# Kernel optimization log

Measured on AMD Instinct MI355X. Metric: run time of the kernel, lower is better.

Reference implementation:

```python
import jax, jax.numpy as jnp
import numpy as np

B, T, C, H = 4, 2048, 1024, 16
D = C // H  # head dim = 64

def setup_inputs() -> dict:
    key = jax.random.key(0)
    k1, k2, k3 = jax.random.split(key, 3)
    x = jax.random.normal(k1, (B, T, C), dtype=jnp.float32)
    # torch Linear weight [out,in]; store transposed for x @ W
    W_attn = jax.random.normal(k2, (C, 3 * C), dtype=jnp.float32) * (1.0 / np.sqrt(C))
    W_proj = jax.random.normal(k3, (C, C), dtype=jnp.float32) * (1.0 / np.sqrt(C))
    return {"x": x, "W_attn": W_attn, "W_proj": W_proj}

def reference(x, W_attn, W_proj):
    qkv = x @ W_attn                          # [B,T,3C]
    q, k, v = jnp.split(qkv, 3, axis=-1)
    # [B,T,C] -> [B,H,T,D]
    def heads(t):
        return t.reshape(B, T, H, D).transpose(0, 2, 1, 3)
    q, k, v = heads(q), heads(k), heads(v)
    att = jnp.einsum('bhqd,bhkd->bhqk', q, k) * (1.0 / np.sqrt(D))  # [B,H,T,T]
    causal = jnp.tril(jnp.ones((T, T), dtype=bool))
    att = jnp.where(causal[None, None, :, :], att, -jnp.inf)
    att = jax.nn.softmax(att, axis=-1)
    y = jnp.einsum('bhqk,bhkd->bhqd', att, v)  # [B,H,T,D]
    y = y.transpose(0, 2, 1, 3).reshape(B, T, C)
    return y @ W_proj
```

## Files before the change

kernel.cpp:

```cpp
#include <hip/hip_runtime.h>
#include <hip/hip_bf16.h>

#define BB 4
#define TT 2048
#define CC 1024
#define HH 16
#define DD 64
#define MM (BB*TT)

typedef unsigned short u16;
typedef __bf16 bf16x8 __attribute__((ext_vector_type(8)));
typedef __bf16 bf16x4v __attribute__((ext_vector_type(4)));
typedef u16 u16x8 __attribute__((ext_vector_type(8)));
typedef u16 u16x4 __attribute__((ext_vector_type(4)));
typedef float f32x4 __attribute__((ext_vector_type(4)));

__device__ __forceinline__ u16 f2bf(float f) {
  union { float f; unsigned u; } v; v.f = f;
  unsigned u = v.u;
  return (u16)((u + 0x7fffu + ((u >> 16) & 1u)) >> 16);
}
__device__ __forceinline__ float bf2f(u16 s) {
  union { unsigned u; float f; } v; v.u = ((unsigned)s) << 16; return v.f;
}
__device__ __forceinline__ bf16x8 ld_bf16x8(const u16* p) {
  return *reinterpret_cast<const bf16x8*>(p);
}
__device__ __forceinline__ f32x4 zero4() {
  f32x4 z; z[0] = 0.f; z[1] = 0.f; z[2] = 0.f; z[3] = 0.f; return z;
}

__device__ __forceinline__ void gld_lds16(const u16* g, u16* l) {
  __builtin_amdgcn_global_load_lds(
      (const __attribute__((address_space(1))) void*)g,
      (__attribute__((address_space(3))) void*)l, 16, 0, 0);
}
__device__ __forceinline__ void wait_vm0() { __builtin_amdgcn_s_waitcnt(0x0F70); }

__device__ __forceinline__ float lane_pull(float x, int srclane) {
  int r = __builtin_amdgcn_ds_bpermute(srclane << 2, __builtin_bit_cast(int, x));
  return __builtin_bit_cast(float, r);
}

__global__ void k_cast_bf16(const float* __restrict__ x, u16* __restrict__ o, int n4) {
  int i = blockIdx.x * blockDim.x + threadIdx.x;
  if (i >= n4) return;
  const float4 v = reinterpret_cast<const float4*>(x)[i];
  u16x4 r; r.x = f2bf(v.x); r.y = f2bf(v.y); r.z = f2bf(v.z); r.w = f2bf(v.w);
  reinterpret_cast<u16x4*>(o)[i] = r;
}

__global__ void k_transpose_bf16(const float* __restrict__ W, u16* __restrict__ Wt,
                                 int K, int N) {
  __shared__ float tile[32][33];
  int nb = blockIdx.x * 32, kb = blockIdx.y * 32;
  int tx = threadIdx.x & 31, ty = threadIdx.x >> 5;
  #pragma unroll
  for (int i = ty; i < 32; i += 8)
    tile[i][tx] = W[(size_t)(kb + i) * N + nb + tx];
  __syncthreads();
  #pragma unroll
  for (int i = ty; i < 32; i += 8)
    Wt[(size_t)(nb + i) * K + kb + tx] = f2bf(tile[tx][i]);
}

template<int EPI>
__global__ __launch_bounds__(256, 3)
void k_gemm_bt(const u16* __restrict__ A, const u16* __restrict__ Bt,
               float* __restrict__ outF, u16* __restrict__ qb, u16* __restrict__ kb,
               u16* __restrict__ vt, int N, int K)
{
  __shared__ u16 As[128 * 64];
  __shared__ u16 Bs[128 * 64];
  const int tid  = threadIdx.x;
  const int lane = tid & 63, w = tid >> 6;
  const int l16  = lane & 15, quad = lane >> 4;
  const int wr = w >> 1, wc = w & 1;
  const int m0 = blockIdx.y * 128, n0 = blockIdx.x * 128;
  const int lr8 = lane >> 3, lc8 = lane & 7;

  f32x4 acc[4][4];
  #pragma unroll
  for (int i = 0; i < 4; ++i)
    #pragma unroll
    for (int j = 0; j < 4; ++j) acc[i][j] = zero4();

  for (int k0 = 0; k0 < K; k0 += 64) {
    __syncthreads();
    #pragma unroll
    for (int p = 0; p < 4; ++p) {
      const int row = w * 32 + p * 8 + lr8;
      const int cs  = lc8 ^ (row & 7);
      gld_lds16(A  + (size_t)(m0 + row) * K + k0 + cs * 8, &As[(w * 32 + p * 8) * 64]);
      gld_lds16(Bt + (size_t)(n0 + row) * K + k0 + cs * 8, &Bs[(w * 32 + p * 8) * 64]);
    }
    wait_vm0();
    __syncthreads();
    #pragma unroll
    for (int s = 0; s < 2; ++s) {
      bf16x8 af[4], bfr[4];
      #pragma unroll
      for (int i = 0; i < 4; ++i) {
        int mrow = wr * 64 + i * 16 + l16;
        af[i]  = ld_bf16x8(&As[mrow * 64 + ((s * 4 + quad) ^ (l16 & 7)) * 8]);
        int nrow = wc * 64 + i * 16 + l16;
        bfr[i] = ld_bf16x8(&Bs[nrow * 64 + ((s * 4 + quad) ^ (l16 & 7)) * 8]);
      }
      #pragma unroll
      for (int i = 0; i < 4; ++i)
        #pragma unroll
        for (int j = 0; j < 4; ++j)
          acc[i][j] = __builtin_amdgcn_mfma_f32_16x16x32_bf16(af[i], bfr[j], acc[i][j], 0, 0, 0);
    }
  }

  #pragma unroll
  for (int i = 0; i < 4; ++i) {
    #pragma unroll
    for (int j = 0; j < 4; ++j) {
      const int n = n0 + wc * 64 + j * 16 + l16;
      const int mb = m0 + wr * 64 + i * 16 + quad * 4;
      if (EPI == 0) {
        #pragma unroll
        for (int r = 0; r < 4; ++r)
          outF[(size_t)(mb + r) * N + n] = acc[i][j][r];
      } else {
        const int b = mb >> 11, tb = mb & 2047;
        if (n < CC) {
          const int h = n >> 6, d = n & 63;
          #pragma unroll
          for (int r = 0; r < 4; ++r)
            qb[(((size_t)(b * HH + h) * TT + tb + r) << 6) + d] = f2bf(acc[i][j][r]);
        } else if (n < 2 * CC) {
          const int n2 = n - CC; const int h = n2 >> 6, d = n2 & 63;
          #pragma unroll
          for (int r = 0; r < 4; ++r)
            kb[(((size_t)(b * HH + h) * TT + tb + r) << 6) + d] = f2bf(acc[i][j][r]);
        } else {
          const int n2 = n - 2 * CC; const int h = n2 >> 6, d = n2 & 63;
          u16x4 cv;
          #pragma unroll
          for (int r = 0; r < 4; ++r) cv[r] = f2bf(acc[i][j][r]);
          *reinterpret_cast<u16x4*>(
              vt + ((size_t)(b * HH + h) * DD + d) * TT + tb) = cv;
        }
      }
    }
  }
}

__global__ __launch_bounds__(256, 6)
void k_attn(const u16* __restrict__ qb, const u16* __restrict__ kb,
            const u16* __restrict__ vt, u16* __restrict__ y)
{
  __shared__ u16 Ks[64 * 64];
  __shared__ u16 Vs[64 * 64];
  __shared__ u16 QP[64 * 64];
  const int tid  = threadIdx.x;
  const int lane = tid & 63, w = tid >> 6;
  const int l16  = lane & 15, quad = lane >> 4;
  const int lr8 = lane >> 3, lc8 = lane & 7;

  const int bx = blockIdx.x;
  const int qt = 31 - (bx >> 6);
  const int bh = bx & 63;
  const int h  = bh & 15, b = bh >> 4;

  const u16* qptr = qb + ((size_t)bh * TT + qt * 64) * DD;
  const u16* kptr = kb + (size_t)bh * TT * DD;
  const u16* vptr = vt + (size_t)bh * DD * TT;

  const float qscale = 0.125f * 1.44269504088896340736f;
  #pragma unroll
  for (int p = 0; p < 2; ++p) {
    const int r = w * 16 + p * 8 + lr8;
    u16x8 v = *reinterpret_cast<const u16x8*>(qptr + (size_t)r * DD + lc8 * 8);
    u16x8 o;
    #pragma unroll
    for (int e = 0; e < 8; ++e) o[e] = f2bf(bf2f(v[e]) * qscale);
    *reinterpret_cast<u16x8*>(&QP[r * 64 + (lc8 ^ lr8) * 8]) = o;
  }
  bf16x8 qf[2];
  #pragma unroll
  for (int s = 0; s < 2; ++s)
    qf[s] = ld_bf16x8(&QP[(w * 16 + l16) * 64 + ((s * 4 + quad) ^ (l16 & 7)) * 8]);

  float rsum = 0.f;
  f32x4 O[4];
  #pragma unroll
  for (int j = 0; j < 4; ++j) O[j] = zero4();

  const int ktiles = qt + 1;
  for (int kt = 0; kt < ktiles; ++kt) {
    __syncthreads();
    {
      const u16* kt0 = kptr + (size_t)kt * 64 * DD;
      const u16* vt0 = vptr + kt * 64;
      #pragma unroll
      for (int p = 0; p < 2; ++p) {
        const int row = w * 16 + p * 8 + lr8;
        const int cs  = lc8 ^ lr8;
        gld_lds16(kt0 + (size_t)row * DD + cs * 8, &Ks[(w * 16 + p * 8) * 64]);
        gld_lds16(vt0 + (size_t)row * TT + cs * 8, &Vs[(w * 16 + p * 8) * 64]);
      }
    }
    wait_vm0();
    __syncthreads();

    f32x4 St[4];
    #pragma unroll
    for (int j = 0; j < 4; ++j) St[j] = zero4();
    #pragma unroll
    for (int s = 0; s < 2; ++s) {
      #pragma unroll
      for (int j = 0; j < 4; ++j) {
        bf16x8 kfr = ld_bf16x8(&Ks[(j * 16 + l16) * 64 + ((s * 4 + quad) ^ (l16 & 7)) * 8]);
        St[j] = __builtin_amdgcn_mfma_f32_16x16x32_bf16(kfr, qf[s], St[j], 0, 0, 0);
      }
    }
    if (kt == qt) {
      const int qg = w * 16 + l16;
      #pragma unroll
      for (int j = 0; j < 4; ++j)
        #pragma unroll
        for (int r = 0; r < 4; ++r)
          if (j * 16 + quad * 4 + r > qg) St[j][r] = -__builtin_inff();
    }

    #pragma unroll
    for (int j = 0; j < 4; ++j)
      #pragma unroll
      for (int r = 0; r < 4; ++r) {
        float p = __builtin_amdgcn_exp2f(St[j][r]);
        St[j][r] = p;
        rsum += p;
      }

    #pragma unroll
    for (int j = 0; j < 4; ++j) {
      union { bf16x4v bv; u16x4 u; } cv;
      cv.bv[0] = (__bf16)St[j][0]; cv.bv[1] = (__bf16)St[j][1];
      cv.bv[2] = (__bf16)St[j][2]; cv.bv[3] = (__bf16)St[j][3];
      const int c = j * 2 + (quad >> 1);
      const int off = w * 1024 + l16 * 64 + ((c ^ (l16 & 7)) << 3) + ((quad & 1) << 2);
      *reinterpret_cast<u16x4*>(&QP[off]) = cv.u;
    }
    #pragma unroll
    for (int s = 0; s < 2; ++s) {
      bf16x8 pf = ld_bf16x8(&QP[w * 1024 + l16 * 64 + ((s * 4 + quad) ^ (l16 & 7)) * 8]);
      #pragma unroll
      for (int j = 0; j < 4; ++j) {
        bf16x8 vf = ld_bf16x8(&Vs[(j * 16 + l16) * 64 + ((s * 4 + quad) ^ (l16 & 7)) * 8]);
        O[j] = __builtin_amdgcn_mfma_f32_16x16x32_bf16(pf, vf, O[j], 0, 0, 0);
      }
    }
  }

  rsum += __shfl_xor(rsum, 16);
  rsum += __shfl_xor(rsum, 32);
  const float linv = 1.0f / rsum;
  f32x4 lv;
  #pragma unroll
  for (int r = 0; r < 4; ++r) lv[r] = lane_pull(linv, quad * 4 + r);
  #pragma unroll
  for (int j = 0; j < 4; ++j) {
    O[j] *= lv;
    #pragma unroll
    for (int r = 0; r < 4; ++r) {
      int t  = qt * 64 + w * 16 + quad * 4 + r;
      int ch = h * 64 + j * 16 + l16;
      y[(size_t)(b * TT + t) * CC + ch] = f2bf(O[j][r]);
    }
  }
}

extern "C" void kernel_launch(void* const* d_in, const int* in_sizes, int n_in,
                              void* d_out, int out_size, void* d_ws, size_t ws_size,
                              hipStream_t stream) {
  const float* x  = (const float*)d_in[0];
  const float* Wa = (const float*)d_in[1];
  const float* Wp = (const float*)d_in[2];
  float* out = (float*)d_out;

  u16* ws   = (u16*)d_ws;
  u16* xb   = ws;
  u16* Wab  = xb   + (size_t)MM * CC;
  u16* Wpb  = Wab  + (size_t)3 * CC * CC;
  u16* qbuf = Wpb  + (size_t)CC * CC;
  u16* kbuf = qbuf + (size_t)MM * CC;
  u16* vtb  = kbuf + (size_t)MM * CC;
  u16* yb   = vtb  + (size_t)MM * CC;

  k_cast_bf16<<<(MM * CC / 4) / 256, 256, 0, stream>>>(x, xb, MM * CC / 4);
  k_transpose_bf16<<<dim3(3 * CC / 32, CC / 32), 256, 0, stream>>>(Wa, Wab, CC, 3 * CC);
  k_transpose_bf16<<<dim3(CC / 32, CC / 32), 256, 0, stream>>>(Wp, Wpb, CC, CC);
  k_gemm_bt<1><<<dim3(3 * CC / 128, MM / 128), 256, 0, stream>>>(
      xb, Wab, nullptr, qbuf, kbuf, vtb, 3 * CC, CC);
  k_attn<<<64 * 32, 256, 0, stream>>>(qbuf, kbuf, vtb, yb);
  k_gemm_bt<0><<<dim3(CC / 128, MM / 128), 256, 0, stream>>>(
      yb, Wpb, out, nullptr, nullptr, nullptr, CC, CC);
}
```

Before: 237.3 us.

## Load 128-key K/V tiles per attention iteration and merge prep kernels

The attention kernel now stages 128 keys of K and V^T into LDS per outer iteration and runs two 64-key sub-steps, so it needs half as many barriers and load waits per query tile. Sub-steps that lie entirely past the causal diagonal are skipped. The LDS footprint grows and launch bounds drop from 6 to 4 blocks per CU, which can reduce occupancy. Separately, the x cast and the two weight transposes are fused into a single prep launch to save launch overhead.

```diff
diff --git a/kernel.cpp b/kernel.cpp
--- a/kernel.cpp
+++ b/kernel.cpp
@@ -42,19 +42,25 @@
   return __builtin_bit_cast(float, r);
 }
 
-__global__ void k_cast_bf16(const float* __restrict__ x, u16* __restrict__ o, int n4) {
-  int i = blockIdx.x * blockDim.x + threadIdx.x;
-  if (i >= n4) return;
-  const float4 v = reinterpret_cast<const float4*>(x)[i];
-  u16x4 r; r.x = f2bf(v.x); r.y = f2bf(v.y); r.z = f2bf(v.z); r.w = f2bf(v.w);
-  reinterpret_cast<u16x4*>(o)[i] = r;
-}
-
-__global__ void k_transpose_bf16(const float* __restrict__ W, u16* __restrict__ Wt,
-                                 int K, int N) {
+#define NC4B ((MM * CC / 4) / 256)
+__global__ void k_prep(const float* __restrict__ x, u16* __restrict__ xb,
+                       const float* __restrict__ Wa, u16* __restrict__ Wab,
+                       const float* __restrict__ Wp, u16* __restrict__ Wpb) {
   __shared__ float tile[32][33];
-  int nb = blockIdx.x * 32, kb = blockIdx.y * 32;
-  int tx = threadIdx.x & 31, ty = threadIdx.x >> 5;
+  const int bx = blockIdx.x;
+  if (bx < NC4B) {
+    int i = bx * 256 + threadIdx.x;
+    const float4 v = reinterpret_cast<const float4*>(x)[i];
+    u16x4 r; r.x = f2bf(v.x); r.y = f2bf(v.y); r.z = f2bf(v.z); r.w = f2bf(v.w);
+    reinterpret_cast<u16x4*>(xb)[i] = r;
+    return;
+  }
+  const float* W; u16* Wt; int K, N, b2;
+  if (bx < NC4B + 3072) { W = Wa; Wt = Wab; K = CC; N = 3 * CC; b2 = bx - NC4B; }
+  else                  { W = Wp; Wt = Wpb; K = CC; N = CC;     b2 = bx - NC4B - 3072; }
+  const int nblk = N / 32;
+  const int nb = (b2 % nblk) * 32, kb = (b2 / nblk) * 32;
+  const int tx = threadIdx.x & 31, ty = threadIdx.x >> 5;
   #pragma unroll
   for (int i = ty; i < 32; i += 8)
     tile[i][tx] = W[(size_t)(kb + i) * N + nb + tx];
@@ -149,12 +155,12 @@
   }
 }
 
-__global__ __launch_bounds__(256, 6)
+__global__ __launch_bounds__(256, 4)
 void k_attn(const u16* __restrict__ qb, const u16* __restrict__ kb,
             const u16* __restrict__ vt, u16* __restrict__ y)
 {
-  __shared__ u16 Ks[64 * 64];
-  __shared__ u16 Vs[64 * 64];
+  __shared__ u16 Ks[128 * 64];
+  __shared__ u16 Vs[64 * 128];
   __shared__ u16 QP[64 * 64];
   const int tid  = threadIdx.x;
   const int lane = tid & 63, w = tid >> 6;
@@ -190,68 +196,83 @@
   #pragma unroll
   for (int j = 0; j < 4; ++j) O[j] = zero4();
 
-  const int ktiles = qt + 1;
-  for (int kt = 0; kt < ktiles; ++kt) {
+  const int qend = qt * 64;
+  const int nkt  = (qt >> 1) + 1;
+  for (int kt = 0; kt < nkt; ++kt) {
     __syncthreads();
     {
-      const u16* kt0 = kptr + (size_t)kt * 64 * DD;
-      const u16* vt0 = vptr + kt * 64;
+      const u16* kt0 = kptr + (size_t)kt * 128 * DD;
       #pragma unroll
-      for (int p = 0; p < 2; ++p) {
-        const int row = w * 16 + p * 8 + lr8;
-        const int cs  = lc8 ^ lr8;
-        gld_lds16(kt0 + (size_t)row * DD + cs * 8, &Ks[(w * 16 + p * 8) * 64]);
-        gld_lds16(vt0 + (size_t)row * TT + cs * 8, &Vs[(w * 16 + p * 8) * 64]);
+      for (int p = 0; p < 4; ++p) {
+        const int row = w * 32 + p * 8 + lr8;
+        const int cs  = lc8 ^ (row & 7);
+        gld_lds16(kt0 + (size_t)row * DD + cs * 8, &Ks[(w * 32 + p * 8) * 64]);
+      }
+      #pragma unroll
+      for (int p = 0; p < 4; ++p) {
+        const int d  = w * 16 + p * 4 + (lane >> 4);
+        const int cs = (lane & 15) ^ (d & 7);
+        gld_lds16(vptr + (size_t)d * TT + kt * 128 + cs * 8,
+                  &Vs[(w * 16 + p * 4) * 128]);
       }
     }
     wait_vm0();
     __syncthreads();
 
-    f32x4 St[4];
-    #pragma unroll
-    for (int j = 0; j < 4; ++j) St[j] = zero4();
-    #pragma unroll
-    for (int s = 0; s < 2; ++s) {
-      #pragma unroll
-      for (int j = 0; j < 4; ++j) {
-        bf16x8 kfr = ld_bf16x8(&Ks[(j * 16 + l16) * 64 + ((s * 4 + quad) ^ (l16 & 7)) * 8]);
-        St[j] = __builtin_amdgcn_mfma_f32_16x16x32_bf16(kfr, qf[s], St[j], 0, 0, 0);
-      }
-    }
-    if (kt == qt) {
-      const int qg = w * 16 + l16;
-      #pragma unroll
-      for (int j = 0; j < 4; ++j)
-        #pragma unroll
-        for (int r = 0; r < 4; ++r)
-          if (j * 16 + quad * 4 + r > qg) St[j][r] = -__builtin_inff();
-    }
-
-    #pragma unroll
-    for (int j = 0; j < 4; ++j)
-      #pragma unroll
-      for (int r = 0; r < 4; ++r) {
-        float p = __builtin_amdgcn_exp2f(St[j][r]);
-        St[j][r] = p;
-        rsum += p;
-      }
-
-    #pragma unroll
-    for (int j = 0; j < 4; ++j) {
-      union { bf16x4v bv; u16x4 u; } cv;
-      cv.bv[0] = (__bf16)St[j][0]; cv.bv[1] = (__bf16)St[j][1];
-      cv.bv[2] = (__bf16)St[j][2]; cv.bv[3] = (__bf16)St[j][3];
-      const int c = j * 2 + (quad >> 1);
-      const int off = w * 1024 + l16 * 64 + ((c ^ (l16 & 7)) << 3) + ((quad & 1) << 2);
-      *reinterpret_cast<u16x4*>(&QP[off]) = cv.u;
-    }
-    #pragma unroll
-    for (int s = 0; s < 2; ++s) {
-      bf16x8 pf = ld_bf16x8(&QP[w * 1024 + l16 * 64 + ((s * 4 + quad) ^ (l16 & 7)) * 8]);
-      #pragma unroll
-      for (int j = 0; j < 4; ++j) {
-        bf16x8 vf = ld_bf16x8(&Vs[(j * 16 + l16) * 64 + ((s * 4 + quad) ^ (l16 & 7)) * 8]);
-        O[j] = __builtin_amdgcn_mfma_f32_16x16x32_bf16(pf, vf, O[j], 0, 0, 0);
+    #pragma unroll
+    for (int h2 = 0; h2 < 2; ++h2) {
+      const int k0 = kt * 128 + h2 * 64;
+      if (k0 <= qend) {
+        f32x4 St[4];
+        #pragma unroll
+        for (int j = 0; j < 4; ++j) St[j] = zero4();
+        #pragma unroll
+        for (int s = 0; s < 2; ++s) {
+          #pragma unroll
+          for (int j = 0; j < 4; ++j) {
+            bf16x8 kfr = ld_bf16x8(&Ks[(h2 * 64 + j * 16 + l16) * 64 +
+                                       ((s * 4 + quad) ^ (l16 & 7)) * 8]);
+            St[j] = __builtin_amdgcn_mfma_f32_16x16x32_bf16(kfr, qf[s], St[j], 0, 0, 0);
+          }
+        }
+        if (k0 == qend) {
+          const int qg = w * 16 + l16;
+          #pragma unroll
+          for (int j = 0; j < 4; ++j)
+            #pragma unroll
+            for (int r = 0; r < 4; ++r)
+              if (j * 16 + quad * 4 + r > qg) St[j][r] = -__builtin_inff();
+        }
+
+        #pragma unroll
+        for (int j = 0; j < 4; ++j)
+          #pragma unroll
+          for (int r = 0; r < 4; ++r) {
+            float p = __builtin_amdgcn_exp2f(St[j][r]);
+            St[j][r] = p;
+            rsum += p;
+          }
+
+        #pragma unroll
+        for (int j = 0; j < 4; ++j) {
+          union { bf16x4v bv; u16x4 u; } cv;
+          cv.bv[0] = (__bf16)St[j][0]; cv.bv[1] = (__bf16)St[j][1];
+          cv.bv[2] = (__bf16)St[j][2]; cv.bv[3] = (__bf16)St[j][3];
+          const int c = j * 2 + (quad >> 1);
+          const int off = w * 1024 + l16 * 64 + ((c ^ (l16 & 7)) << 3) + ((quad & 1) << 2);
+          *reinterpret_cast<u16x4*>(&QP[off]) = cv.u;
+        }
+        #pragma unroll
+        for (int s = 0; s < 2; ++s) {
+          bf16x8 pf = ld_bf16x8(&QP[w * 1024 + l16 * 64 +
+                                    ((s * 4 + quad) ^ (l16 & 7)) * 8]);
+          #pragma unroll
+          for (int j = 0; j < 4; ++j) {
+            bf16x8 vf = ld_bf16x8(&Vs[(j * 16 + l16) * 128 +
+                                      ((h2 * 8 + s * 4 + quad) ^ (l16 & 7)) * 8]);
+            O[j] = __builtin_amdgcn_mfma_f32_16x16x32_bf16(pf, vf, O[j], 0, 0, 0);
+          }
+        }
       }
     }
   }
@@ -291,9 +312,7 @@
   u16* vtb  = kbuf + (size_t)MM * CC;
   u16* yb   = vtb  + (size_t)MM * CC;
 
-  k_cast_bf16<<<(MM * CC / 4) / 256, 256, 0, stream>>>(x, xb, MM * CC / 4);
-  k_transpose_bf16<<<dim3(3 * CC / 32, CC / 32), 256, 0, stream>>>(Wa, Wab, CC, 3 * CC);
-  k_transpose_bf16<<<dim3(CC / 32, CC / 32), 256, 0, stream>>>(Wp, Wpb, CC, CC);
+  k_prep<<<NC4B + 3072 + 1024, 256, 0, stream>>>(x, xb, Wa, Wab, Wp, Wpb);
   k_gemm_bt<1><<<dim3(3 * CC / 128, MM / 128), 256, 0, stream>>>(
       xb, Wab, nullptr, qbuf, kbuf, vtb, 3 * CC, CC);
   k_attn<<<64 * 32, 256, 0, stream>>>(qbuf, kbuf, vtb, yb);
```

New measurement: 231.2 us. -2.6%, faster.
